# Kernel tuning notes

Measured on AMD Instinct MI355X. Metric: run time of the kernel, lower is better.

Reference implementation:

```python
import jax, jax.numpy as jnp
import numpy as np

N = 50000        # nodes
E = 1_600_000    # edges
G = 64           # graphs in batch
IN = 10          # raw node feature width
XS, XE = 4, 10   # bus slice -> in_dim = 6
H = 256          # hidden_dim
OUT = 256        # out_dim
L = 3            # n_layers per expert
NE = 8           # n_experts
K = 2            # top_k


def _w(key, shape):
    fan_in = shape[-2] if len(shape) > 1 else shape[-1]
    return jax.random.normal(key, shape, jnp.float32) / np.sqrt(fan_in).astype(np.float32)


def setup_inputs() -> dict:
    key = jax.random.key(0)
    ks = jax.random.split(key, 18)
    x = jax.random.normal(ks[0], (N, IN), jnp.float32)
    edge_index = jax.random.randint(ks[1], (2, E), 0, N, dtype=jnp.int32)
    batch = jnp.sort(jax.random.randint(ks[2], (N,), 0, G, dtype=jnp.int32))
    return {
        "x": x,
        "edge_index": edge_index,
        "batch": batch,
        # SharedBusEncoder: Linear(in_dim, hidden) + ReLU
        "W_enc": _w(ks[3], (XE - XS, H)), "b_enc": jnp.zeros((H,), jnp.float32),
        # semantic BaseRouter: Linear(H,H)+ReLU+Linear(H,NE)
        "Ws1": _w(ks[4], (H, H)), "bs1": jnp.zeros((H,), jnp.float32),
        "Ws2": _w(ks[5], (H, NE)), "bs2": jnp.zeros((NE,), jnp.float32),
        # structural BaseRouter: Linear(2,H)+ReLU+Linear(H,NE)
        "Wt1": _w(ks[6], (2, H)), "bt1": jnp.zeros((H,), jnp.float32),
        "Wt2": _w(ks[7], (H, NE)), "bt2": jnp.zeros((NE,), jnp.float32),
        # GraphConvExpert stacks: x' = x@W_self + (sum_neighbors x)@W_neigh + b
        "W_self": _w(ks[8], (NE, L, H, OUT)),
        "W_neigh": _w(ks[9], (NE, L, H, OUT)),
        "b_exp": jnp.zeros((NE, L, OUT), jnp.float32),
    }


def reference(x, edge_index, batch, W_enc, b_enc, Ws1, bs1, Ws2, bs2,
              Wt1, bt1, Wt2, bt2, W_self, W_neigh, b_exp):
    src, dst = edge_index[0], edge_index[1]

    # SharedBusEncoder on bus feature slice
    h = jax.nn.relu(x[:, XS:XE] @ W_enc + b_enc)                       # [N, H]

    # graph_size_features: per-graph log node/edge counts, broadcast to nodes
    nodes_per_g = jax.ops.segment_sum(jnp.ones((N,), jnp.float32), batch, G)
    edges_per_g = jax.ops.segment_sum(jnp.ones((E,), jnp.float32), batch[src], G)
    size_feat = jnp.stack([jnp.log1p(nodes_per_g), jnp.log1p(edges_per_g)], -1)[batch]  # [N, 2]

    # dual routers, averaged
    sem = jax.nn.relu(h @ Ws1 + bs1) @ Ws2 + bs2                       # [N, NE]
    stru = jax.nn.relu(size_feat @ Wt1 + bt1) @ Wt2 + bt2              # [N, NE]
    logits = 0.5 * sem + 0.5 * stru

    # sparse_routing: softmax -> top-k mask -> renormalize (eval path, no noise)
    probs = jax.nn.softmax(logits, axis=-1)
    _, topi = jax.lax.top_k(probs, K)                                  # [N, K]
    mask = jnp.zeros_like(probs).at[jnp.arange(N)[:, None], topi].set(1.0)
    sp = probs * mask
    sparse = sp / jnp.sum(sp, axis=-1, keepdims=True)                  # [N, NE]

    # dense GraphConv experts over all nodes
    def run_expert(Ws, Wn, b):
        z = h
        for l in range(L):
            agg = jax.ops.segment_sum(z[src], dst, N)                  # neighbor sum
            z = z @ Ws[l] + agg @ Wn[l] + b[l]
            if l < L - 1:
                z = jax.nn.relu(z)
        return z                                                        # [N, OUT]

    y = jax.vmap(run_expert)(W_self, W_neigh, b_exp)                   # [NE, N, OUT]
    return jnp.einsum('end,ne->nd', y, sparse)                         # [N, OUT]
```

## Files before the change

kernel.cpp:

```cpp
#include <hip/hip_runtime.h>


#define NN 50000
#define EE 1600000
#define GG 64
#define HH 256
#define NEXP 8
#define LAY 3
#define KD 512
#define MT 128
#define BK 64
#define GB 391
#define SLG 6256
#define MPAD 50048L

typedef __attribute__((ext_vector_type(8))) short bf16x8;
typedef __attribute__((ext_vector_type(8))) unsigned short u16x8;
typedef __attribute__((ext_vector_type(4))) float f32x4;

__device__ __forceinline__ float bf2f(unsigned short u) {
    union { unsigned int i; float f; } v; v.i = ((unsigned int)u) << 16; return v.f;
}
__device__ __forceinline__ unsigned short f2bf(float f) {
    union { unsigned int i; float f; } v; v.f = f;
    unsigned int r = (v.i + 0x7FFFu + ((v.i >> 16) & 1u)) >> 16;
    return (unsigned short)r;
}
__device__ __forceinline__ void gll16(unsigned short* l, const unsigned short* g) {
    __builtin_amdgcn_global_load_lds((__attribute__((address_space(1))) void*)g,
                                     (__attribute__((address_space(3))) void*)l, 16, 0, 0);
}

__global__ void encoder_kernel(const float* __restrict__ x, const float* __restrict__ W,
                               const float* __restrict__ b, unsigned short* __restrict__ out) {
    int n = blockIdx.x, j = threadIdx.x;
    float acc = b[j];
#pragma unroll
    for (int i = 0; i < 6; i++) acc += x[n * 10 + 4 + i] * W[i * HH + j];
    acc = fmaxf(acc, 0.f);
    out[(long)n * KD + j] = f2bf(acc);
}

__global__ void pack_experts(const float* __restrict__ Wself, const float* __restrict__ Wneigh,
                             unsigned short* __restrict__ Bt) {
    int idx = blockIdx.x * 256 + threadIdx.x;
    int n = idx & 255; int r = idx >> 8;
    int k = r & 511; r >>= 9;
    int l = r % LAY; int e = r / LAY;
    float v = (k < 256) ? Wself[(((e * LAY + l) * HH) + k) * HH + n]
                        : Wneigh[(((e * LAY + l) * HH) + (k - 256)) * HH + n];
    Bt[(((long)(e * LAY + l) * HH + n) * KD) + k] = f2bf(v);
}

__global__ void pack_ws1(const float* __restrict__ W, unsigned short* __restrict__ Bt) {
    int idx = blockIdx.x * 256 + threadIdx.x;
    int n = idx & 255; int k = idx >> 8;
    Bt[(long)n * HH + k] = f2bf(W[k * HH + n]);
}

__global__ void degp_kernel(const int* __restrict__ dst, int* __restrict__ deg,
                            unsigned short* __restrict__ perm) {
    int e = blockIdx.x * 256 + threadIdx.x;
    if (e < EE) perm[e] = (unsigned short)atomicAdd(&deg[dst[e]], 1);
}

#define HBLK 128
#define HITER ((EE + HBLK * 256 - 1) / (HBLK * 256))
__global__ void hist2_kernel(const int* __restrict__ src, const int* __restrict__ batch,
                             int* __restrict__ ecnt) {
    __shared__ int h[GG];
    if (threadIdx.x < GG) h[threadIdx.x] = 0;
    __syncthreads();
    int lane = threadIdx.x & 63;
    int gid = blockIdx.x * 256 + threadIdx.x;
    int cnt = 0;
    for (int it = 0; it < HITER; it++) {
        long e = (long)it * (HBLK * 256) + gid;
        int g = (e < EE) ? batch[src[e]] : -1;
        for (int gg = 0; gg < GG; gg++) {
            unsigned long long m = __ballot(g == gg);
            if (lane == gg) cnt += (int)__popcll(m);
        }
    }
    atomicAdd(&h[lane], cnt);
    __syncthreads();
    if (threadIdx.x < GG && h[threadIdx.x]) atomicAdd(&ecnt[threadIdx.x], h[threadIdx.x]);
}

__global__ void stru_kernel(const int* __restrict__ batch, const int* __restrict__ ecnt,
                            const float* __restrict__ Wt1, const float* __restrict__ bt1,
                            const float* __restrict__ Wt2, const float* __restrict__ bt2,
                            float* __restrict__ strug) {
    __shared__ float t[HH];
    __shared__ int nc;
    int g = blockIdx.x, j = threadIdx.x;
    if (j == 0) {
        int lo = 0, hi = NN;
        while (lo < hi) { int mid = (lo + hi) >> 1; if (batch[mid] < g) lo = mid + 1; else hi = mid; }
        int s = lo; lo = 0; hi = NN;
        while (lo < hi) { int mid = (lo + hi) >> 1; if (batch[mid] < g + 1) lo = mid + 1; else hi = mid; }
        nc = lo - s;
    }
    __syncthreads();
    float nf = log1pf((float)nc);
    float ef = log1pf((float)ecnt[g]);
    float v = nf * Wt1[j] + ef * Wt1[HH + j] + bt1[j];
    t[j] = fmaxf(v, 0.f);
    __syncthreads();
    if (j < 8) {
        float sum = bt2[j];
        for (int k = 0; k < HH; k++) sum += t[k] * Wt2[k * 8 + j];
        strug[g * 8 + j] = sum;
    }
}

__global__ void scan_kernel(const int* __restrict__ deg, int* __restrict__ rowstart) {
    __shared__ int wsum[16];
    __shared__ int carry_s;
    int tid = threadIdx.x;
    int wid = tid >> 6, lane = tid & 63;
    if (tid == 0) carry_s = 0;
    __syncthreads();
    for (int base = 0; base < NN; base += 1024) {
        int i = base + tid;
        int v = (i < NN) ? deg[i] : 0;
        int sc = v;
#pragma unroll
        for (int off = 1; off < 64; off <<= 1) {
            int t = __shfl_up(sc, off, 64);
            if (lane >= off) sc += t;
        }
        if (lane == 63) wsum[wid] = sc;
        __syncthreads();
        int carry = carry_s;
        int prev = 0;
        for (int w = 0; w < wid; w++) prev += wsum[w];
        int excl = carry + prev + sc - v;
        if (i < NN) rowstart[i] = excl;
        __syncthreads();
        if (tid == 1023) carry_s = carry + prev + sc;
    }
    __syncthreads();
    if (tid == 0) rowstart[NN] = carry_s;
}

__global__ void scatter2_kernel(const int* __restrict__ src, const int* __restrict__ dst,
                                const unsigned short* __restrict__ perm,
                                const int* __restrict__ rowstart,
                                unsigned short* __restrict__ cols) {
    int e = blockIdx.x * 256 + threadIdx.x;
    if (e < EE) cols[rowstart[dst[e]] + (int)perm[e]] = (unsigned short)src[e];
}

__global__ void agg_kernel(unsigned short* __restrict__ base, long estride,
                           const int* __restrict__ rowstart, const unsigned short* __restrict__ cols,
                           const int* __restrict__ listp, const int* __restrict__ cntp) {
    unsigned short* Z = base + (long)blockIdx.y * estride;
    const int slice = blockIdx.x & 7;
    const int chunk = blockIdx.x >> 3;
    const int grp = threadIdx.x >> 2, l4 = threadIdx.x & 3;
    int limit = cntp ? cntp[blockIdx.y] : NN;
    if (chunk * 64 >= limit) return;
    int idx = chunk * 64 + grp;
    if (idx >= limit) return;
    int nid = listp ? (listp[(long)blockIdx.y * NN + idx] & 0xFFFF) : idx;
    int s = rowstart[nid], e = rowstart[nid + 1];
    const int co = slice * 32 + l4 * 8;
    float acc[8] = {0.f, 0.f, 0.f, 0.f, 0.f, 0.f, 0.f, 0.f};
    int i = s;
    for (; i + 8 <= e; i += 8) {
        int c[8];
#pragma unroll
        for (int u = 0; u < 8; u++) c[u] = (int)cols[i + u];
        u16x8 v[8];
#pragma unroll
        for (int u = 0; u < 8; u++) v[u] = *(const u16x8*)&Z[(long)c[u] * KD + co];
#pragma unroll
        for (int u = 0; u < 8; u++)
#pragma unroll
            for (int j = 0; j < 8; j++) acc[j] += bf2f(v[u][j]);
    }
    for (; i < e; i++) {
        int c = (int)cols[i];
        u16x8 v = *(const u16x8*)&Z[(long)c * KD + co];
#pragma unroll
        for (int j = 0; j < 8; j++) acc[j] += bf2f(v[j]);
    }
    u16x8 o;
#pragma unroll
    for (int j = 0; j < 8; j++) o[j] = f2bf(acc[j]);
    *(u16x8*)&Z[(long)nid * KD + 256 + co] = o;
}

__global__ void route_kernel(const unsigned short* __restrict__ T, const float* __restrict__ Ws2,
                             const float* __restrict__ bs2, const float* __restrict__ strug,
                             const int* __restrict__ batch, float* __restrict__ sparse,
                             int* __restrict__ topi) {
    int nid = blockIdx.x * 4 + (threadIdx.x >> 6);
    if (nid >= NN) return;
    int lane = threadIdx.x & 63;
    float s[8];
#pragma unroll
    for (int j = 0; j < 8; j++) s[j] = 0.f;
    ushort4 t4 = *(const ushort4*)&T[(long)nid * HH + lane * 4];
    float tv[4] = { bf2f(t4.x), bf2f(t4.y), bf2f(t4.z), bf2f(t4.w) };
#pragma unroll
    for (int kk = 0; kk < 4; kk++) {
        int k = lane * 4 + kk;
#pragma unroll
        for (int j = 0; j < 8; j++) s[j] += tv[kk] * Ws2[k * 8 + j];
    }
#pragma unroll
    for (int off = 32; off >= 1; off >>= 1) {
#pragma unroll
        for (int j = 0; j < 8; j++) s[j] += __shfl_xor(s[j], off, 64);
    }
    int g = batch[nid];
    float p[8], mx = -1e30f;
#pragma unroll
    for (int j = 0; j < 8; j++) {
        p[j] = 0.5f * (s[j] + bs2[j] + strug[g * 8 + j]);
        mx = fmaxf(mx, p[j]);
    }
    float ex[8];
#pragma unroll
    for (int j = 0; j < 8; j++) ex[j] = expf(p[j] - mx);
    int i1 = 0;
#pragma unroll
    for (int j = 1; j < 8; j++) if (ex[j] > ex[i1]) i1 = j;
    int i2 = (i1 == 0) ? 1 : 0;
#pragma unroll
    for (int j = 0; j < 8; j++) if (j != i1 && ex[j] > ex[i2]) i2 = j;
    float r = 1.f / (ex[i1] + ex[i2]);
    if (lane == 0) topi[nid] = i1 | (i2 << 8);
    if (lane < 8)
        sparse[(long)nid * 8 + lane] = (lane == i1) ? ex[i1] * r : (lane == i2) ? ex[i2] * r : 0.f;
}

__global__ void build_lists(const float* __restrict__ sparse, const int* __restrict__ topi,
                            int* __restrict__ cnt, int* __restrict__ lists) {
    __shared__ int lc[NEXP], lb[NEXP];
    int tid = threadIdx.x;
    if (tid < NEXP) lc[tid] = 0;
    __syncthreads();
    int n = blockIdx.x * 256 + tid;
    int le_[2], pk_[2], ps_[2];
    int cc = 0;
    if (n < NN) {
        int t1 = topi[n] & 0xFF;
#pragma unroll
        for (int e = 0; e < NEXP; e++) {
            if (sparse[(long)n * 8 + e] > 0.f && cc < 2) {
                le_[cc] = e;
                pk_[cc] = n | ((e == t1) ? 0 : (1 << 16));
                ps_[cc] = atomicAdd(&lc[e], 1);
                cc++;
            }
        }
    }
    __syncthreads();
    if (tid < NEXP) lb[tid] = atomicAdd(&cnt[tid], lc[tid]);
    __syncthreads();
    for (int c = 0; c < cc; c++)
        lists[(long)le_[c] * NN + lb[le_[c]] + ps_[c]] = pk_[c];
}

template <int MODE>
__global__ __launch_bounds__(256, 2) void gemm_kernel(
    const unsigned short* __restrict__ A, long ae, int lda, int K,
    const unsigned short* __restrict__ Bt, long bte,
    const float* __restrict__ bias, int be_s,
    void* __restrict__ outp, long oe, int ldz,
    const float* __restrict__ sparse, int e0,
    const int* __restrict__ listp, const int* __restrict__ cntp) {
    __shared__ __align__(16) unsigned short Alds[MT * 64];
    __shared__ __align__(16) unsigned short Blds[HH * 64];
    __shared__ int nodeids[MT];
    const int el = blockIdx.y;
    const unsigned short* Ae = A + (long)el * ae;
    const unsigned short* Bte = Bt + (long)el * bte;
    const float* be = bias + (long)el * be_s;
    const int tid = threadIdx.x;
    const int wave = tid >> 6, lane = tid & 63;
    const int m = lane & 15, q = lane >> 4;
    const long row0 = (long)blockIdx.x * MT;

    if constexpr (MODE == 1) {
        int limit = cntp[el];
        if (row0 >= limit) return;
        if (tid < MT) {
            long rr = row0 + tid;
            nodeids[tid] = (rr < limit) ? listp[(long)el * NN + rr] : -1;
        }
        __syncthreads();
    }

    const unsigned short* asrc[4];
#pragma unroll
    for (int i = 0; i < 4; i++) {
        int slot = tid + 256 * i;
        int r = slot >> 3, cg = (slot & 7) ^ (r & 7);
        long arow;
        if constexpr (MODE == 0) {
            arow = row0 + r;
        } else {
            int v = nodeids[r];
            arow = (v >= 0) ? (v & 0xFFFF) : 0;
        }
        asrc[i] = Ae + arow * (long)lda + cg * 8;
    }
    const unsigned short* bsrc[8];
#pragma unroll
    for (int i = 0; i < 8; i++) {
        int slot = tid + 256 * i;
        int r = slot >> 3, cg = (slot & 7) ^ (r & 7);
        bsrc[i] = Bte + (long)r * K + cg * 8;
    }

    f32x4 acc[2][16];
#pragma unroll
    for (int i = 0; i < 2; i++)
#pragma unroll
        for (int j = 0; j < 16; j++) acc[i][j] = (f32x4){0.f, 0.f, 0.f, 0.f};

    const int swz = (m & 7) << 3;
    for (int k0 = 0; k0 < K; k0 += BK) {
#pragma unroll
        for (int i = 0; i < 4; i++) gll16(&Alds[(tid + 256 * i) * 8], asrc[i] + k0);
#pragma unroll
        for (int i = 0; i < 8; i++) gll16(&Blds[(tid + 256 * i) * 8], bsrc[i] + k0);
        __syncthreads();
#pragma unroll
        for (int kk = 0; kk < BK; kk += 32) {
            const int ch8 = (((kk >> 3) + q) << 3) ^ swz;
            const int ao = (wave * 32 + m) * 64 + ch8;
            bf16x8 a0 = *(const bf16x8*)&Alds[ao];
            bf16x8 a1 = *(const bf16x8*)&Alds[ao + 16 * 64];
#pragma unroll
            for (int ct = 0; ct < 16; ct++) {
                bf16x8 b = *(const bf16x8*)&Blds[(ct * 16 + m) * 64 + ch8];
                acc[0][ct] = __builtin_amdgcn_mfma_f32_16x16x32_bf16(a0, b, acc[0][ct], 0, 0, 0);
                acc[1][ct] = __builtin_amdgcn_mfma_f32_16x16x32_bf16(a1, b, acc[1][ct], 0, 0, 0);
            }
        }
        __syncthreads();
    }
#pragma unroll
    for (int mt = 0; mt < 2; mt++) {
        int rtile = wave * 32 + mt * 16 + q * 4;
        if constexpr (MODE == 0) {
            unsigned short* oute = (unsigned short*)outp + (long)el * oe;
            long rbase = row0 + rtile;
#pragma unroll
            for (int ct = 0; ct < 16; ct++) {
                int col = ct * 16 + m;
                float bv = be[col];
#pragma unroll
                for (int r = 0; r < 4; r++) {
                    long grow = rbase + r;
                    if (grow < NN) {
                        float v = fmaxf(acc[mt][ct][r] + bv, 0.f);
                        oute[grow * ldz + col] = f2bf(v);
                    }
                }
            }
        } else {
            unsigned short* outR = (unsigned short*)outp;
            int v4[4]; float w4[4];
#pragma unroll
            for (int r = 0; r < 4; r++) {
                v4[r] = nodeids[rtile + r];
                w4[r] = (v4[r] >= 0) ? sparse[(long)(v4[r] & 0xFFFF) * 8 + e0 + el] : 0.f;
            }
#pragma unroll
            for (int ct = 0; ct < 16; ct++) {
                int col = ct * 16 + m;
                float bv = be[col];
#pragma unroll
                for (int r = 0; r < 4; r++) {
                    if (v4[r] >= 0) {
                        long nid = v4[r] & 0xFFFF;
                        long rank = (v4[r] >> 16) & 1;
                        outR[(rank * MPAD + nid) * HH + col] = f2bf(w4[r] * (acc[mt][ct][r] + bv));
                    }
                }
            }
        }
    }
}

__global__ void combine_kernel(const unsigned short* __restrict__ outR, float* __restrict__ out) {
    long base = ((long)blockIdx.x * 256 + threadIdx.x) * 8;
    u16x8 r0 = *(const u16x8*)&outR[base];
    u16x8 r1 = *(const u16x8*)&outR[MPAD * HH + base];
    f32x4 lo, hi;
#pragma unroll
    for (int j = 0; j < 4; j++) lo[j] = bf2f(r0[j]) + bf2f(r1[j]);
#pragma unroll
    for (int j = 0; j < 4; j++) hi[j] = bf2f(r0[j + 4]) + bf2f(r1[j + 4]);
    *(f32x4*)&out[base] = lo;
    *(f32x4*)&out[base + 4] = hi;
}

extern "C" void kernel_launch(void* const* d_in, const int* in_sizes, int n_in,
                              void* d_out, int out_size, void* d_ws, size_t ws_size,
                              hipStream_t stream) {
    const float* x     = (const float*)d_in[0];
    const int*   ei    = (const int*)d_in[1];
    const int*   src   = ei;
    const int*   dst   = ei + EE;
    const int*   batch = (const int*)d_in[2];
    const float* W_enc = (const float*)d_in[3];
    const float* b_enc = (const float*)d_in[4];
    const float* Ws1   = (const float*)d_in[5];
    const float* bs1   = (const float*)d_in[6];
    const float* Ws2   = (const float*)d_in[7];
    const float* bs2   = (const float*)d_in[8];
    const float* Wt1   = (const float*)d_in[9];
    const float* bt1   = (const float*)d_in[10];
    const float* Wt2   = (const float*)d_in[11];
    const float* bt2   = (const float*)d_in[12];
    const float* W_self  = (const float*)d_in[13];
    const float* W_neigh = (const float*)d_in[14];
    const float* b_exp   = (const float*)d_in[15];
    float* out = (float*)d_out;

    char* ws = (char*)d_ws;
    size_t off = 0;
    auto alloc = [&](size_t b) { size_t p = off; off = (off + b + 255) & ~(size_t)255; return ws + p; };

    unsigned short* Ash  = (unsigned short*)alloc((size_t)MPAD * KD * 2);
    unsigned short* outR = (unsigned short*)alloc((size_t)2 * MPAD * HH * 2);
    unsigned short* Tbuf = outR;
    unsigned short* BtE = (unsigned short*)alloc((size_t)NEXP * LAY * HH * KD * 2);
    unsigned short* Bt1 = (unsigned short*)alloc((size_t)HH * HH * 2);
    float* sparse  = (float*)alloc((size_t)NN * 8 * 4);
    int* topi      = (int*)alloc((size_t)NN * 4);
    float* strug   = (float*)alloc((size_t)GG * 8 * 4);
    int* ecnt      = (int*)alloc((size_t)GG * 4);
    int* deg       = (int*)alloc((size_t)NN * 4);
    int* rowstart  = (int*)alloc((size_t)(NN + 1) * 4);
    unsigned short* perm = (unsigned short*)alloc((size_t)EE * 2);
    unsigned short* cols = (unsigned short*)alloc((size_t)EE * 2);
    int* lists     = (int*)alloc((size_t)NEXP * NN * 4);
    int* cnt8      = (int*)alloc((size_t)NEXP * 4);

    const long BUFS = MPAD * KD;
    long avail = ((long)ws_size - (long)off) / (BUFS * 2);
    int EG = (avail < 1) ? 1 : (avail > NEXP ? NEXP : (int)avail);
    unsigned short* bufs = (unsigned short*)(ws + off);

    hipMemsetAsync(ecnt, 0, GG * 4, stream);
    hipMemsetAsync(deg, 0, (size_t)NN * 4, stream);
    hipMemsetAsync(cnt8, 0, NEXP * 4, stream);

    pack_experts<<<NEXP * LAY * KD * HH / 256, 256, 0, stream>>>(W_self, W_neigh, BtE);
    pack_ws1<<<HH * HH / 256, 256, 0, stream>>>(Ws1, Bt1);
    encoder_kernel<<<NN, HH, 0, stream>>>(x, W_enc, b_enc, Ash);

    degp_kernel<<<(EE + 255) / 256, 256, 0, stream>>>(dst, deg, perm);
    hist2_kernel<<<HBLK, 256, 0, stream>>>(src, batch, ecnt);
    scan_kernel<<<1, 1024, 0, stream>>>(deg, rowstart);
    scatter2_kernel<<<(EE + 255) / 256, 256, 0, stream>>>(src, dst, perm, rowstart, cols);
    stru_kernel<<<GG, HH, 0, stream>>>(batch, ecnt, Wt1, bt1, Wt2, bt2, strug);

    gemm_kernel<0><<<dim3(GB, 1), 256, 0, stream>>>(Ash, 0, KD, HH, Bt1, 0, bs1, 0,
                                                    Tbuf, 0, HH, nullptr, 0, nullptr, nullptr);
    route_kernel<<<(NN + 3) / 4, 256, 0, stream>>>(Tbuf, Ws2, bs2, strug, batch, sparse, topi);
    build_lists<<<(NN + 255) / 256, 256, 0, stream>>>(sparse, topi, cnt8, lists);

    agg_kernel<<<dim3(SLG, 1), 256, 0, stream>>>(Ash, 0, rowstart, cols, nullptr, nullptr);

    const long BTL = (long)LAY * HH * KD;
    for (int e0 = 0; e0 < NEXP; e0 += EG) {
        int eg = (NEXP - e0 < EG) ? (NEXP - e0) : EG;
        dim3 gg(GB, eg), ga(SLG, eg);
        gemm_kernel<0><<<gg, 256, 0, stream>>>(Ash, 0, KD, KD,
                                               BtE + (size_t)(e0 * LAY + 0) * HH * KD, BTL,
                                               b_exp + (size_t)e0 * LAY * HH, LAY * HH,
                                               bufs, BUFS, KD, nullptr, 0, nullptr, nullptr);
        agg_kernel<<<ga, 256, 0, stream>>>(bufs, BUFS, rowstart, cols, nullptr, nullptr);
        gemm_kernel<0><<<gg, 256, 0, stream>>>(bufs, BUFS, KD, KD,
                                               BtE + (size_t)(e0 * LAY + 1) * HH * KD, BTL,
                                               b_exp + (size_t)e0 * LAY * HH + HH, LAY * HH,
                                               bufs, BUFS, KD, nullptr, 0, nullptr, nullptr);
        agg_kernel<<<ga, 256, 0, stream>>>(bufs, BUFS, rowstart, cols,
                                           lists + (size_t)e0 * NN, cnt8 + e0);
        gemm_kernel<1><<<gg, 256, 0, stream>>>(bufs, BUFS, KD, KD,
                                               BtE + (size_t)(e0 * LAY + 2) * HH * KD, BTL,
                                               b_exp + (size_t)e0 * LAY * HH + 2 * HH, LAY * HH,
                                               outR, 0, 0, sparse, e0,
                                               lists + (size_t)e0 * NN, cnt8 + e0);
    }
    combine_kernel<<<NN * HH / 8 / 256, 256, 0, stream>>>(outR, out);
}
```

Measured before the change: 2.597 ms.

## Restructure neighbor aggregation: half-wave per node, full-row reads, prefetched indices

The aggregation kernel now gives each node a 32-lane half-wave that covers all 256 hidden columns with 16-byte loads, replacing the old split into eight column slices spread across blocks. This cuts repeated index reads and gives each gather a contiguous 512-byte row segment. Neighbor indices are read 16 at a time and the next batch is prefetched while the current gathers run. Padded entries are masked with a zero weight instead of a scalar tail loop, which costs extra work on nodes whose degree is not a multiple of 16.

Measured after the change: 2.245 ms. 1.16x faster.

```diff
diff --git a/kernel.cpp b/kernel.cpp
--- a/kernel.cpp
+++ b/kernel.cpp
@@ -11,7 +11,7 @@
 #define MT 128
 #define BK 64
 #define GB 391
-#define SLG 6256
+#define AGB 6250
 #define MPAD 50048L
 
 typedef __attribute__((ext_vector_type(8))) short bf16x8;
@@ -156,40 +156,47 @@
                            const int* __restrict__ rowstart, const unsigned short* __restrict__ cols,
                            const int* __restrict__ listp, const int* __restrict__ cntp) {
     unsigned short* Z = base + (long)blockIdx.y * estride;
-    const int slice = blockIdx.x & 7;
-    const int chunk = blockIdx.x >> 3;
-    const int grp = threadIdx.x >> 2, l4 = threadIdx.x & 3;
+    int half = threadIdx.x >> 5;
+    int lane = threadIdx.x & 31;
+    int idx = blockIdx.x * 8 + half;
     int limit = cntp ? cntp[blockIdx.y] : NN;
-    if (chunk * 64 >= limit) return;
-    int idx = chunk * 64 + grp;
     if (idx >= limit) return;
     int nid = listp ? (listp[(long)blockIdx.y * NN + idx] & 0xFFFF) : idx;
     int s = rowstart[nid], e = rowstart[nid + 1];
-    const int co = slice * 32 + l4 * 8;
+    const unsigned short* Zl = Z + lane * 8;
     float acc[8] = {0.f, 0.f, 0.f, 0.f, 0.f, 0.f, 0.f, 0.f};
-    int i = s;
-    for (; i + 8 <= e; i += 8) {
-        int c[8];
-#pragma unroll
-        for (int u = 0; u < 8; u++) c[u] = (int)cols[i + u];
-        u16x8 v[8];
-#pragma unroll
-        for (int u = 0; u < 8; u++) v[u] = *(const u16x8*)&Z[(long)c[u] * KD + co];
-#pragma unroll
-        for (int u = 0; u < 8; u++)
-#pragma unroll
-            for (int j = 0; j < 8; j++) acc[j] += bf2f(v[u][j]);
-    }
-    for (; i < e; i++) {
-        int c = (int)cols[i];
-        u16x8 v = *(const u16x8*)&Z[(long)c * KD + co];
-#pragma unroll
-        for (int j = 0; j < 8; j++) acc[j] += bf2f(v[j]);
+    int c[16];
+#pragma unroll
+    for (int u = 0; u < 16; u++) {
+        int ii = s + u;
+        int cl = (ii < EE) ? ii : (EE - 1);
+        c[u] = (ii < e) ? (int)cols[cl] : 0;
+    }
+    for (int i = s; i < e; i += 16) {
+        u16x8 v[16];
+#pragma unroll
+        for (int u = 0; u < 16; u++) v[u] = *(const u16x8*)&Zl[(long)c[u] * KD];
+        int cn[16];
+        int ib = i + 16;
+#pragma unroll
+        for (int u = 0; u < 16; u++) {
+            int ii = ib + u;
+            int cl = (ii < EE) ? ii : (EE - 1);
+            cn[u] = (ii < e) ? (int)cols[cl] : 0;
+        }
+#pragma unroll
+        for (int u = 0; u < 16; u++) {
+            float w = (i + u < e) ? 1.f : 0.f;
+#pragma unroll
+            for (int j = 0; j < 8; j++) acc[j] = fmaf(w, bf2f(v[u][j]), acc[j]);
+        }
+#pragma unroll
+        for (int u = 0; u < 16; u++) c[u] = cn[u];
     }
     u16x8 o;
 #pragma unroll
     for (int j = 0; j < 8; j++) o[j] = f2bf(acc[j]);
-    *(u16x8*)&Z[(long)nid * KD + 256 + co] = o;
+    *(u16x8*)&Z[(long)nid * KD + 256 + lane * 8] = o;
 }
 
 __global__ void route_kernel(const unsigned short* __restrict__ T, const float* __restrict__ Ws2,
@@ -469,12 +476,12 @@
     route_kernel<<<(NN + 3) / 4, 256, 0, stream>>>(Tbuf, Ws2, bs2, strug, batch, sparse, topi);
     build_lists<<<(NN + 255) / 256, 256, 0, stream>>>(sparse, topi, cnt8, lists);
 
-    agg_kernel<<<dim3(SLG, 1), 256, 0, stream>>>(Ash, 0, rowstart, cols, nullptr, nullptr);
+    agg_kernel<<<dim3(AGB, 1), 256, 0, stream>>>(Ash, 0, rowstart, cols, nullptr, nullptr);
 
     const long BTL = (long)LAY * HH * KD;
     for (int e0 = 0; e0 < NEXP; e0 += EG) {
         int eg = (NEXP - e0 < EG) ? (NEXP - e0) : EG;
-        dim3 gg(GB, eg), ga(SLG, eg);
+        dim3 gg(GB, eg), ga(AGB, eg);
         gemm_kernel<0><<<gg, 256, 0, stream>>>(Ash, 0, KD, KD,
                                                BtE + (size_t)(e0 * LAY + 0) * HH * KD, BTL,
                                                b_exp + (size_t)e0 * LAY * HH, LAY * HH,
```

## Sort nodes by degree for aggregation and assign one half-wave per node row

Applied to the files above, without the earlier changes.

Adds a counting sort of nodes by descending in-degree (histogram, scan, scatter) and makes the aggregation kernel and the expert lists follow that order, so waves process nodes of similar degree and load imbalance shrinks. The aggregation kernel is also remapped so 32 lanes cover a whole 256-wide feature row per node instead of 4 lanes over 32-column slices. This trades three small extra kernels and an indirection through the order array for more uniform per-wave work and fully coalesced row gathers.

After: 2.374 ms. -8.6%, faster.

```diff
diff --git a/kernel.cpp b/kernel.cpp
--- a/kernel.cpp
+++ b/kernel.cpp
@@ -11,8 +11,9 @@
 #define MT 128
 #define BK 64
 #define GB 391
-#define SLG 6256
+#define AGB 6250
 #define MPAD 50048L
+#define DBIN 128
 
 typedef __attribute__((ext_vector_type(8))) short bf16x8;
 typedef __attribute__((ext_vector_type(8))) unsigned short u16x8;
@@ -85,6 +86,29 @@
     atomicAdd(&h[lane], cnt);
     __syncthreads();
     if (threadIdx.x < GG && h[threadIdx.x]) atomicAdd(&ecnt[threadIdx.x], h[threadIdx.x]);
+}
+
+__global__ void dhist_kernel(const int* __restrict__ deg, int* __restrict__ dh) {
+    int n = blockIdx.x * 256 + threadIdx.x;
+    if (n < NN) {
+        int d = deg[n]; if (d > DBIN - 1) d = DBIN - 1;
+        atomicAdd(&dh[(DBIN - 1) - d], 1);
+    }
+}
+__global__ void dscan_kernel(const int* __restrict__ dh, int* __restrict__ dcur) {
+    if (threadIdx.x == 0) {
+        int run = 0;
+        for (int i = 0; i < DBIN; i++) { dcur[i] = run; run += dh[i]; }
+    }
+}
+__global__ void dorder_kernel(const int* __restrict__ deg, int* __restrict__ dcur,
+                              int* __restrict__ order) {
+    int n = blockIdx.x * 256 + threadIdx.x;
+    if (n < NN) {
+        int d = deg[n]; if (d > DBIN - 1) d = DBIN - 1;
+        int p = atomicAdd(&dcur[(DBIN - 1) - d], 1);
+        order[p] = n;
+    }
 }
 
 __global__ void stru_kernel(const int* __restrict__ batch, const int* __restrict__ ecnt,
@@ -154,18 +178,16 @@
 
 __global__ void agg_kernel(unsigned short* __restrict__ base, long estride,
                            const int* __restrict__ rowstart, const unsigned short* __restrict__ cols,
-                           const int* __restrict__ listp, const int* __restrict__ cntp) {
+                           const int* __restrict__ listp, long lstride,
+                           const int* __restrict__ cntp) {
     unsigned short* Z = base + (long)blockIdx.y * estride;
-    const int slice = blockIdx.x & 7;
-    const int chunk = blockIdx.x >> 3;
-    const int grp = threadIdx.x >> 2, l4 = threadIdx.x & 3;
+    int half = threadIdx.x >> 5;
+    int lane = threadIdx.x & 31;
+    int idx = blockIdx.x * 8 + half;
     int limit = cntp ? cntp[blockIdx.y] : NN;
-    if (chunk * 64 >= limit) return;
-    int idx = chunk * 64 + grp;
     if (idx >= limit) return;
-    int nid = listp ? (listp[(long)blockIdx.y * NN + idx] & 0xFFFF) : idx;
+    int nid = listp ? (listp[lstride * blockIdx.y + idx] & 0xFFFF) : idx;
     int s = rowstart[nid], e = rowstart[nid + 1];
-    const int co = slice * 32 + l4 * 8;
     float acc[8] = {0.f, 0.f, 0.f, 0.f, 0.f, 0.f, 0.f, 0.f};
     int i = s;
     for (; i + 8 <= e; i += 8) {
@@ -174,7 +196,7 @@
         for (int u = 0; u < 8; u++) c[u] = (int)cols[i + u];
         u16x8 v[8];
 #pragma unroll
-        for (int u = 0; u < 8; u++) v[u] = *(const u16x8*)&Z[(long)c[u] * KD + co];
+        for (int u = 0; u < 8; u++) v[u] = *(const u16x8*)&Z[(long)c[u] * KD + lane * 8];
 #pragma unroll
         for (int u = 0; u < 8; u++)
 #pragma unroll
@@ -182,14 +204,14 @@
     }
     for (; i < e; i++) {
         int c = (int)cols[i];
-        u16x8 v = *(const u16x8*)&Z[(long)c * KD + co];
+        u16x8 v = *(const u16x8*)&Z[(long)c * KD + lane * 8];
 #pragma unroll
         for (int j = 0; j < 8; j++) acc[j] += bf2f(v[j]);
     }
     u16x8 o;
 #pragma unroll
     for (int j = 0; j < 8; j++) o[j] = f2bf(acc[j]);
-    *(u16x8*)&Z[(long)nid * KD + 256 + co] = o;
+    *(u16x8*)&Z[(long)nid * KD + 256 + lane * 8] = o;
 }
 
 __global__ void route_kernel(const unsigned short* __restrict__ T, const float* __restrict__ Ws2,
@@ -238,15 +260,17 @@
 }
 
 __global__ void build_lists(const float* __restrict__ sparse, const int* __restrict__ topi,
+                            const int* __restrict__ order,
                             int* __restrict__ cnt, int* __restrict__ lists) {
     __shared__ int lc[NEXP], lb[NEXP];
     int tid = threadIdx.x;
     if (tid < NEXP) lc[tid] = 0;
     __syncthreads();
-    int n = blockIdx.x * 256 + tid;
+    int gid = blockIdx.x * 256 + tid;
+    int n = (gid < NN) ? order[gid] : -1;
     int le_[2], pk_[2], ps_[2];
     int cc = 0;
-    if (n < NN) {
+    if (n >= 0) {
         int t1 = topi[n] & 0xFF;
 #pragma unroll
         for (int e = 0; e < NEXP; e++) {
@@ -444,6 +468,9 @@
     unsigned short* cols = (unsigned short*)alloc((size_t)EE * 2);
     int* lists     = (int*)alloc((size_t)NEXP * NN * 4);
     int* cnt8      = (int*)alloc((size_t)NEXP * 4);
+    int* order     = (int*)alloc((size_t)NN * 4);
+    int* dh        = (int*)alloc((size_t)DBIN * 4);
+    int* dcur      = (int*)alloc((size_t)DBIN * 4);
 
     const long BUFS = MPAD * KD;
     long avail = ((long)ws_size - (long)off) / (BUFS * 2);
@@ -453,6 +480,7 @@
     hipMemsetAsync(ecnt, 0, GG * 4, stream);
     hipMemsetAsync(deg, 0, (size_t)NN * 4, stream);
     hipMemsetAsync(cnt8, 0, NEXP * 4, stream);
+    hipMemsetAsync(dh, 0, DBIN * 4, stream);
 
     pack_experts<<<NEXP * LAY * KD * HH / 256, 256, 0, stream>>>(W_self, W_neigh, BtE);
     pack_ws1<<<HH * HH / 256, 256, 0, stream>>>(Ws1, Bt1);
@@ -462,30 +490,33 @@
     hist2_kernel<<<HBLK, 256, 0, stream>>>(src, batch, ecnt);
     scan_kernel<<<1, 1024, 0, stream>>>(deg, rowstart);
     scatter2_kernel<<<(EE + 255) / 256, 256, 0, stream>>>(src, dst, perm, rowstart, cols);
+    dhist_kernel<<<(NN + 255) / 256, 256, 0, stream>>>(deg, dh);
+    dscan_kernel<<<1, 64, 0, stream>>>(dh, dcur);
+    dorder_kernel<<<(NN + 255) / 256, 256, 0, stream>>>(deg, dcur, order);
     stru_kernel<<<GG, HH, 0, stream>>>(batch, ecnt, Wt1, bt1, Wt2, bt2, strug);
 
     gemm_kernel<0><<<dim3(GB, 1), 256, 0, stream>>>(Ash, 0, KD, HH, Bt1, 0, bs1, 0,
                                                     Tbuf, 0, HH, nullptr, 0, nullptr, nullptr);
     route_kernel<<<(NN + 3) / 4, 256, 0, stream>>>(Tbuf, Ws2, bs2, strug, batch, sparse, topi);
-    build_lists<<<(NN + 255) / 256, 256, 0, stream>>>(sparse, topi, cnt8, lists);
-
-    agg_kernel<<<dim3(SLG, 1), 256, 0, stream>>>(Ash, 0, rowstart, cols, nullptr, nullptr);
+    build_lists<<<(NN + 255) / 256, 256, 0, stream>>>(sparse, topi, order, cnt8, lists);
+
+    agg_kernel<<<dim3(AGB, 1), 256, 0, stream>>>(Ash, 0, rowstart, cols, order, 0L, nullptr);
 
     const long BTL = (long)LAY * HH * KD;
     for (int e0 = 0; e0 < NEXP; e0 += EG) {
         int eg = (NEXP - e0 < EG) ? (NEXP - e0) : EG;
-        dim3 gg(GB, eg), ga(SLG, eg);
+        dim3 gg(GB, eg), ga(AGB, eg);
         gemm_kernel<0><<<gg, 256, 0, stream>>>(Ash, 0, KD, KD,
                                                BtE + (size_t)(e0 * LAY + 0) * HH * KD, BTL,
                                                b_exp + (size_t)e0 * LAY * HH, LAY * HH,
                                                bufs, BUFS, KD, nullptr, 0, nullptr, nullptr);
-        agg_kernel<<<ga, 256, 0, stream>>>(bufs, BUFS, rowstart, cols, nullptr, nullptr);
+        agg_kernel<<<ga, 256, 0, stream>>>(bufs, BUFS, rowstart, cols, order, 0L, nullptr);
         gemm_kernel<0><<<gg, 256, 0, stream>>>(bufs, BUFS, KD, KD,
                                                BtE + (size_t)(e0 * LAY + 1) * HH * KD, BTL,
                                                b_exp + (size_t)e0 * LAY * HH + HH, LAY * HH,
                                                bufs, BUFS, KD, nullptr, 0, nullptr, nullptr);
         agg_kernel<<<ga, 256, 0, stream>>>(bufs, BUFS, rowstart, cols,
-                                           lists + (size_t)e0 * NN, cnt8 + e0);
+                                           lists + (size_t)e0 * NN, (long)NN, cnt8 + e0);
         gemm_kernel<1><<<gg, 256, 0, stream>>>(bufs, BUFS, KD, KD,
                                                BtE + (size_t)(e0 * LAY + 2) * HH * KD, BTL,
                                                b_exp + (size_t)e0 * LAY * HH + 2 * HH, LAY * HH,
```

## Sort CSR neighbor lists and give each node a 32-lane row-wide aggregation

Applied to the files above, without the earlier changes.

Adds a per-row insertion sort of the CSR column indices so neighbor gathers walk source rows in ascending address order. The aggregation kernel is remapped so 32 lanes cover a node's full 256-wide feature row (8 nodes per block) instead of splitting each row across 8 column-slice blocks. Whole-row access gives coalesced 512-byte reads per neighbor and avoids re-reading the CSR list in 8 separate blocks. It costs an extra serial sort kernel, and uneven degrees within a wavefront can cause divergence.

Result: faster. 2.348 ms (-9.6%).

```diff
diff --git a/kernel.cpp b/kernel.cpp
--- a/kernel.cpp
+++ b/kernel.cpp
@@ -11,7 +11,7 @@
 #define MT 128
 #define BK 64
 #define GB 391
-#define SLG 6256
+#define AGB 6250
 #define MPAD 50048L
 
 typedef __attribute__((ext_vector_type(8))) short bf16x8;
@@ -152,20 +152,29 @@
     if (e < EE) cols[rowstart[dst[e]] + (int)perm[e]] = (unsigned short)src[e];
 }
 
+__global__ void sortrow_kernel(const int* __restrict__ rowstart, unsigned short* __restrict__ cols) {
+    int n = blockIdx.x * 256 + threadIdx.x;
+    if (n >= NN) return;
+    int s = rowstart[n], e = rowstart[n + 1];
+    for (int i = s + 1; i < e; i++) {
+        unsigned short key = cols[i];
+        int j = i - 1;
+        while (j >= s && cols[j] > key) { cols[j + 1] = cols[j]; j--; }
+        cols[j + 1] = key;
+    }
+}
+
 __global__ void agg_kernel(unsigned short* __restrict__ base, long estride,
                            const int* __restrict__ rowstart, const unsigned short* __restrict__ cols,
                            const int* __restrict__ listp, const int* __restrict__ cntp) {
     unsigned short* Z = base + (long)blockIdx.y * estride;
-    const int slice = blockIdx.x & 7;
-    const int chunk = blockIdx.x >> 3;
-    const int grp = threadIdx.x >> 2, l4 = threadIdx.x & 3;
+    int half = threadIdx.x >> 5;
+    int lane = threadIdx.x & 31;
+    int idx = blockIdx.x * 8 + half;
     int limit = cntp ? cntp[blockIdx.y] : NN;
-    if (chunk * 64 >= limit) return;
-    int idx = chunk * 64 + grp;
     if (idx >= limit) return;
     int nid = listp ? (listp[(long)blockIdx.y * NN + idx] & 0xFFFF) : idx;
     int s = rowstart[nid], e = rowstart[nid + 1];
-    const int co = slice * 32 + l4 * 8;
     float acc[8] = {0.f, 0.f, 0.f, 0.f, 0.f, 0.f, 0.f, 0.f};
     int i = s;
     for (; i + 8 <= e; i += 8) {
@@ -174,7 +183,7 @@
         for (int u = 0; u < 8; u++) c[u] = (int)cols[i + u];
         u16x8 v[8];
 #pragma unroll
-        for (int u = 0; u < 8; u++) v[u] = *(const u16x8*)&Z[(long)c[u] * KD + co];
+        for (int u = 0; u < 8; u++) v[u] = *(const u16x8*)&Z[(long)c[u] * KD + lane * 8];
 #pragma unroll
         for (int u = 0; u < 8; u++)
 #pragma unroll
@@ -182,14 +191,14 @@
     }
     for (; i < e; i++) {
         int c = (int)cols[i];
-        u16x8 v = *(const u16x8*)&Z[(long)c * KD + co];
+        u16x8 v = *(const u16x8*)&Z[(long)c * KD + lane * 8];
 #pragma unroll
         for (int j = 0; j < 8; j++) acc[j] += bf2f(v[j]);
     }
     u16x8 o;
 #pragma unroll
     for (int j = 0; j < 8; j++) o[j] = f2bf(acc[j]);
-    *(u16x8*)&Z[(long)nid * KD + 256 + co] = o;
+    *(u16x8*)&Z[(long)nid * KD + 256 + lane * 8] = o;
 }
 
 __global__ void route_kernel(const unsigned short* __restrict__ T, const float* __restrict__ Ws2,
@@ -462,6 +471,7 @@
     hist2_kernel<<<HBLK, 256, 0, stream>>>(src, batch, ecnt);
     scan_kernel<<<1, 1024, 0, stream>>>(deg, rowstart);
     scatter2_kernel<<<(EE + 255) / 256, 256, 0, stream>>>(src, dst, perm, rowstart, cols);
+    sortrow_kernel<<<(NN + 255) / 256, 256, 0, stream>>>(rowstart, cols);
     stru_kernel<<<GG, HH, 0, stream>>>(batch, ecnt, Wt1, bt1, Wt2, bt2, strug);
 
     gemm_kernel<0><<<dim3(GB, 1), 256, 0, stream>>>(Ash, 0, KD, HH, Bt1, 0, bs1, 0,
@@ -469,12 +479,12 @@
     route_kernel<<<(NN + 3) / 4, 256, 0, stream>>>(Tbuf, Ws2, bs2, strug, batch, sparse, topi);
     build_lists<<<(NN + 255) / 256, 256, 0, stream>>>(sparse, topi, cnt8, lists);
 
-    agg_kernel<<<dim3(SLG, 1), 256, 0, stream>>>(Ash, 0, rowstart, cols, nullptr, nullptr);
+    agg_kernel<<<dim3(AGB, 1), 256, 0, stream>>>(Ash, 0, rowstart, cols, nullptr, nullptr);
 
     const long BTL = (long)LAY * HH * KD;
     for (int e0 = 0; e0 < NEXP; e0 += EG) {
         int eg = (NEXP - e0 < EG) ? (NEXP - e0) : EG;
-        dim3 gg(GB, eg), ga(SLG, eg);
+        dim3 gg(GB, eg), ga(AGB, eg);
         gemm_kernel<0><<<gg, 256, 0, stream>>>(Ash, 0, KD, KD,
                                                BtE + (size_t)(e0 * LAY + 0) * HH * KD, BTL,
                                                b_exp + (size_t)e0 * LAY * HH, LAY * HH,
```
